# Kernel tuning notes

Measured on AMD Instinct MI355X. Metric: run time of the kernel, lower is better.

The kernel has to match this reference:

```python
import jax, jax.numpy as jnp
import numpy as np

B, T, C, H = 4096, 96, 256, 64  # batch, seq (<= BLOCK_SIZE=96), N_EMBED, head_size


def setup_inputs() -> dict:
    key = jax.random.key(0)
    k1, k2, k3, k4 = jax.random.split(key, 4)
    x = jax.random.normal(k1, (B, T, C), dtype=jnp.float32)
    # nn.Linear(C, H, bias=False) stores W as [H, C]; we keep [C, H] so y = x @ W.
    scale = 1.0 / jnp.sqrt(C)
    Wk = jax.random.normal(k2, (C, H), dtype=jnp.float32) * scale
    Wq = jax.random.normal(k3, (C, H), dtype=jnp.float32) * scale
    Wv = jax.random.normal(k4, (C, H), dtype=jnp.float32) * scale
    return {"x": x, "Wk": Wk, "Wq": Wq, "Wv": Wv}


def reference(x, Wk, Wq, Wv):
    Bx, Tx, Cx = x.shape
    k = x @ Wk                      # [B, T, H]
    q = x @ Wq                      # [B, T, H]
    v = x @ Wv                      # [B, T, H]
    # NOTE: original scales by C**-0.5 (embed dim), not head_size**-0.5.
    wei = jnp.einsum('bth,bsh->bts', q, k) * (Cx ** -0.5)  # [B, T, T]
    causal = jnp.tril(jnp.ones((Tx, Tx), dtype=bool))
    wei = jnp.where(causal, wei, -jnp.inf)
    wei = jax.nn.softmax(wei, axis=-1)
    # dropout is identity at eval time
    return jnp.einsum('bts,bsh->bth', wei, v)  # [B, T, H]
```

## Files before the change

### kernel.cpp

```cpp
#include <hip/hip_runtime.h>
#include <cstddef>


typedef __bf16 bf16x8 __attribute__((ext_vector_type(8)));
typedef float f32x4 __attribute__((ext_vector_type(4)));

static __device__ __forceinline__ unsigned short f2bf_u16(float f) {
  union { float f; unsigned int u; } c; c.f = f;
  return (unsigned short)((c.u + 0x7FFFu + ((c.u >> 16) & 1u)) >> 16);
}

__global__ void pack_w(const float* __restrict__ Wk, const float* __restrict__ Wq,
                       const float* __restrict__ Wv, unsigned short* __restrict__ pack) {
  int idx = blockIdx.x * blockDim.x + threadIdx.x;
  int lane = idx & 63;
  int t = idx >> 6;
  int nt = t & 3; t >>= 2;
  int kt = t & 7; t >>= 3;
  int p  = t;
  if (p >= 3) return;
  const float* W = (p == 0) ? Wk : (p == 1) ? Wq : Wv;
  int k0 = kt * 32 + (lane >> 4) * 8;
  int n  = nt * 16 + (lane & 15);
  unsigned short* dst = pack + (size_t)idx * 8;
#pragma unroll
  for (int j = 0; j < 8; ++j) dst[j] = f2bf_u16(W[(size_t)(k0 + j) * 64 + n]);
}

#define LDQ 72
#define LDV 104
#define LDP 104

__global__ __launch_bounds__(384, 3) void head_fused(
    const float* __restrict__ x, const unsigned short* __restrict__ pack,
    float* __restrict__ out) {
  __shared__ __attribute__((aligned(16))) unsigned short qs [96 * LDQ];
  __shared__ __attribute__((aligned(16))) unsigned short ksm[96 * LDQ];
  __shared__ __attribute__((aligned(16))) unsigned short vTs[64 * LDV];
  __shared__ __attribute__((aligned(16))) unsigned short Ps [96 * LDP];
  __shared__ float rowsum[96];

  const int b    = blockIdx.x;
  const int w    = threadIdx.x >> 6;
  const int lane = threadIdx.x & 63;
  const int lo   = lane & 15;
  const int hi   = lane >> 4;

  const float* __restrict__ xb = x + (size_t)b * (96 * 256);

  f32x4 acc[3][4];
#pragma unroll
  for (int p = 0; p < 3; ++p)
#pragma unroll
    for (int nt = 0; nt < 4; ++nt) acc[p][nt] = (f32x4){0.f, 0.f, 0.f, 0.f};

  const int am = 16 * w + lo;
#pragma unroll 2
  for (int kt = 0; kt < 8; ++kt) {
    const float* src = xb + (size_t)am * 256 + kt * 32 + hi * 8;
    f32x4 a0 = *(const f32x4*)src;
    f32x4 a1 = *(const f32x4*)(src + 4);
    union { bf16x8 v; unsigned short u[8]; } af;
#pragma unroll
    for (int j = 0; j < 4; ++j) { af.u[j] = f2bf_u16(a0[j]); af.u[4 + j] = f2bf_u16(a1[j]); }
#pragma unroll
    for (int p = 0; p < 3; ++p) {
#pragma unroll
      for (int nt = 0; nt < 4; ++nt) {
        bf16x8 bf = *(const bf16x8*)(pack + ((size_t)(((p * 8 + kt) * 4 + nt) * 64 + lane) * 8));
        acc[p][nt] = __builtin_amdgcn_mfma_f32_16x16x32_bf16(af.v, bf, acc[p][nt], 0, 0, 0);
      }
    }
  }
#pragma unroll
  for (int nt = 0; nt < 4; ++nt) {
#pragma unroll
    for (int r = 0; r < 4; ++r) {
      int row = 16 * w + hi * 4 + r;
      int col = 16 * nt + lo;
      ksm[row * LDQ + col] = f2bf_u16(acc[0][nt][r]);
      qs [row * LDQ + col] = f2bf_u16(acc[1][nt][r]);
      vTs[col * LDV + row] = f2bf_u16(acc[2][nt][r]);
    }
  }
  __syncthreads();

  f32x4 sacc[6];
#pragma unroll
  for (int jt = 0; jt < 6; ++jt) sacc[jt] = (f32x4){0.f, 0.f, 0.f, 0.f};

  bf16x8 qf0 = *(const bf16x8*)(qs + (16 * w + lo) * LDQ + hi * 8);
  bf16x8 qf1 = *(const bf16x8*)(qs + (16 * w + lo) * LDQ + 32 + hi * 8);
  for (int jt = 0; jt <= w; ++jt) {
    bf16x8 kf0 = *(const bf16x8*)(ksm + (16 * jt + lo) * LDQ + hi * 8);
    bf16x8 kf1 = *(const bf16x8*)(ksm + (16 * jt + lo) * LDQ + 32 + hi * 8);
    sacc[jt] = __builtin_amdgcn_mfma_f32_16x16x32_bf16(qf0, kf0, sacc[jt], 0, 0, 0);
    sacc[jt] = __builtin_amdgcn_mfma_f32_16x16x32_bf16(qf1, kf1, sacc[jt], 0, 0, 0);
  }

#pragma unroll
  for (int r = 0; r < 4; ++r) {
    int row = 16 * w + hi * 4 + r;
    float pr[6];
    float mx = -1e30f;
    for (int jt = 0; jt <= w; ++jt) {
      int col = 16 * jt + lo;
      float s = sacc[jt][r] * 0.0625f;
      s = (col <= row) ? s : -1e30f;
      pr[jt] = s;
      mx = fmaxf(mx, s);
    }
#pragma unroll
    for (int off = 1; off < 16; off <<= 1) mx = fmaxf(mx, __shfl_xor(mx, off, 64));
    float sum = 0.f;
    for (int jt = 0; jt <= w; ++jt) {
      float p = __expf(pr[jt] - mx);
      pr[jt] = p;
      sum += p;
    }
#pragma unroll
    for (int off = 1; off < 16; off <<= 1) sum += __shfl_xor(sum, off, 64);
#pragma unroll
    for (int jt = 0; jt < 6; ++jt) {
      float p = (jt <= w) ? pr[jt] : 0.f;
      Ps[row * LDP + 16 * jt + lo] = f2bf_u16(p);
    }
    if (lo == 0) rowsum[row] = sum;
  }
  __syncthreads();

  f32x4 oacc[4];
#pragma unroll
  for (int nt = 0; nt < 4; ++nt) oacc[nt] = (f32x4){0.f, 0.f, 0.f, 0.f};

  const int ksmax = (16 * w + 15) >> 5;
  for (int ks = 0; ks <= ksmax; ++ks) {
    bf16x8 pf = *(const bf16x8*)(Ps + (16 * w + lo) * LDP + ks * 32 + hi * 8);
#pragma unroll
    for (int nt = 0; nt < 4; ++nt) {
      bf16x8 vf = *(const bf16x8*)(vTs + (16 * nt + lo) * LDV + ks * 32 + hi * 8);
      oacc[nt] = __builtin_amdgcn_mfma_f32_16x16x32_bf16(pf, vf, oacc[nt], 0, 0, 0);
    }
  }

  float* __restrict__ ob = out + (size_t)b * (96 * 64);
#pragma unroll
  for (int r = 0; r < 4; ++r) {
    int row = 16 * w + hi * 4 + r;
    float inv = 1.0f / rowsum[row];
#pragma unroll
    for (int nt = 0; nt < 4; ++nt) {
      ob[row * 64 + 16 * nt + lo] = oacc[nt][r] * inv;
    }
  }
}

extern "C" void kernel_launch(void* const* d_in, const int* in_sizes, int n_in,
                              void* d_out, int out_size, void* d_ws, size_t ws_size,
                              hipStream_t stream) {
  const float* x  = (const float*)d_in[0];
  const float* Wk = (const float*)d_in[1];
  const float* Wq = (const float*)d_in[2];
  const float* Wv = (const float*)d_in[3];
  float* out = (float*)d_out;
  unsigned short* pack = (unsigned short*)d_ws;

  const int B = in_sizes[0] / (96 * 256);

  pack_w<<<24, 256, 0, stream>>>(Wk, Wq, Wv, pack);
  head_fused<<<B, 384, 0, stream>>>(x, pack, out);
}
```

Before: 689.8 us.

## Split fused attention head into separate QKV-projection and attention kernels

The single fused kernel becomes two launches. The first projects x to Q, K and V, writing Q/K as bf16 into the output buffer and a transposed V into workspace. The second reads them back to compute causal softmax attention. Moving the Q/K/V tiles out of shared memory cuts LDS per block, raising the occupancy bounds (4 and 6 blocks per CU instead of 3) so more memory latency can be hidden. The cost is an extra kernel launch and a global round trip for the intermediates. Reusing the output buffer is safe only because each block reads its own Q/K slice before overwriting it.

Measured after the change: 765.2 us. +10.9%, slower.

```diff
diff --git a/kernel.cpp b/kernel.cpp
--- a/kernel.cpp
+++ b/kernel.cpp
@@ -4,6 +4,7 @@
 
 typedef __bf16 bf16x8 __attribute__((ext_vector_type(8)));
 typedef float f32x4 __attribute__((ext_vector_type(4)));
+typedef unsigned short ushort8 __attribute__((ext_vector_type(8)));
 
 static __device__ __forceinline__ unsigned short f2bf_u16(float f) {
   union { float f; unsigned int u; } c; c.f = f;
@@ -27,18 +28,13 @@
   for (int j = 0; j < 8; ++j) dst[j] = f2bf_u16(W[(size_t)(k0 + j) * 64 + n]);
 }
 
-#define LDQ 72
-#define LDV 104
-#define LDP 104
-
-__global__ __launch_bounds__(384, 3) void head_fused(
+#define LDVA 104
+
+__global__ __launch_bounds__(384, 4) void qkv_kernel(
     const float* __restrict__ x, const unsigned short* __restrict__ pack,
-    float* __restrict__ out) {
-  __shared__ __attribute__((aligned(16))) unsigned short qs [96 * LDQ];
-  __shared__ __attribute__((aligned(16))) unsigned short ksm[96 * LDQ];
-  __shared__ __attribute__((aligned(16))) unsigned short vTs[64 * LDV];
-  __shared__ __attribute__((aligned(16))) unsigned short Ps [96 * LDP];
-  __shared__ float rowsum[96];
+    unsigned short* __restrict__ qk,
+    unsigned short* __restrict__ vT) {
+  __shared__ __attribute__((aligned(16))) unsigned short vTs[64 * LDVA];
 
   const int b    = blockIdx.x;
   const int w    = threadIdx.x >> 6;
@@ -72,28 +68,55 @@
       }
     }
   }
+
+  unsigned short* qb = qk + (size_t)b * 12288;
 #pragma unroll
   for (int nt = 0; nt < 4; ++nt) {
 #pragma unroll
     for (int r = 0; r < 4; ++r) {
       int row = 16 * w + hi * 4 + r;
       int col = 16 * nt + lo;
-      ksm[row * LDQ + col] = f2bf_u16(acc[0][nt][r]);
-      qs [row * LDQ + col] = f2bf_u16(acc[1][nt][r]);
-      vTs[col * LDV + row] = f2bf_u16(acc[2][nt][r]);
+      qb[row * 64 + col]        = f2bf_u16(acc[1][nt][r]);
+      qb[6144 + row * 64 + col] = f2bf_u16(acc[0][nt][r]);
+      vTs[col * LDVA + row]     = f2bf_u16(acc[2][nt][r]);
     }
   }
   __syncthreads();
 
+  unsigned short* vb = vT + (size_t)b * 6144;
+  int h   = threadIdx.x / 6;
+  int seg = threadIdx.x - h * 6;
+  ushort8 s0 = *(const ushort8*)(vTs + h * LDVA + seg * 16);
+  ushort8 s1 = *(const ushort8*)(vTs + h * LDVA + seg * 16 + 8);
+  *(ushort8*)(vb + h * 96 + seg * 16)     = s0;
+  *(ushort8*)(vb + h * 96 + seg * 16 + 8) = s1;
+}
+
+#define LDP 104
+
+__global__ __launch_bounds__(384, 6) void attn_kernel(
+    const unsigned short* qk, const unsigned short* vT, float* out) {
+  __shared__ __attribute__((aligned(16))) unsigned short Ps[96 * LDP];
+  __shared__ float rowsum[96];
+
+  const int b    = blockIdx.x;
+  const int w    = threadIdx.x >> 6;
+  const int lane = threadIdx.x & 63;
+  const int lo   = lane & 15;
+  const int hi   = lane >> 4;
+
+  const unsigned short* qb = qk + (size_t)b * 12288;
+  const unsigned short* kb = qb + 6144;
+
   f32x4 sacc[6];
 #pragma unroll
   for (int jt = 0; jt < 6; ++jt) sacc[jt] = (f32x4){0.f, 0.f, 0.f, 0.f};
 
-  bf16x8 qf0 = *(const bf16x8*)(qs + (16 * w + lo) * LDQ + hi * 8);
-  bf16x8 qf1 = *(const bf16x8*)(qs + (16 * w + lo) * LDQ + 32 + hi * 8);
+  bf16x8 qf0 = *(const bf16x8*)(qb + (16 * w + lo) * 64 + hi * 8);
+  bf16x8 qf1 = *(const bf16x8*)(qb + (16 * w + lo) * 64 + 32 + hi * 8);
   for (int jt = 0; jt <= w; ++jt) {
-    bf16x8 kf0 = *(const bf16x8*)(ksm + (16 * jt + lo) * LDQ + hi * 8);
-    bf16x8 kf1 = *(const bf16x8*)(ksm + (16 * jt + lo) * LDQ + 32 + hi * 8);
+    bf16x8 kf0 = *(const bf16x8*)(kb + (16 * jt + lo) * 64 + hi * 8);
+    bf16x8 kf1 = *(const bf16x8*)(kb + (16 * jt + lo) * 64 + 32 + hi * 8);
     sacc[jt] = __builtin_amdgcn_mfma_f32_16x16x32_bf16(qf0, kf0, sacc[jt], 0, 0, 0);
     sacc[jt] = __builtin_amdgcn_mfma_f32_16x16x32_bf16(qf1, kf1, sacc[jt], 0, 0, 0);
   }
@@ -133,17 +156,18 @@
 #pragma unroll
   for (int nt = 0; nt < 4; ++nt) oacc[nt] = (f32x4){0.f, 0.f, 0.f, 0.f};
 
+  const unsigned short* vb = vT + (size_t)b * 6144;
   const int ksmax = (16 * w + 15) >> 5;
   for (int ks = 0; ks <= ksmax; ++ks) {
     bf16x8 pf = *(const bf16x8*)(Ps + (16 * w + lo) * LDP + ks * 32 + hi * 8);
 #pragma unroll
     for (int nt = 0; nt < 4; ++nt) {
-      bf16x8 vf = *(const bf16x8*)(vTs + (16 * nt + lo) * LDV + ks * 32 + hi * 8);
+      bf16x8 vf = *(const bf16x8*)(vb + (16 * nt + lo) * 96 + ks * 32 + hi * 8);
       oacc[nt] = __builtin_amdgcn_mfma_f32_16x16x32_bf16(pf, vf, oacc[nt], 0, 0, 0);
     }
   }
 
-  float* __restrict__ ob = out + (size_t)b * (96 * 64);
+  float* ob = out + (size_t)b * (96 * 64);
 #pragma unroll
   for (int r = 0; r < 4; ++r) {
     int row = 16 * w + hi * 4 + r;
@@ -163,10 +187,14 @@
   const float* Wq = (const float*)d_in[2];
   const float* Wv = (const float*)d_in[3];
   float* out = (float*)d_out;
+
+  const int B = in_sizes[0] / (96 * 256);
+
   unsigned short* pack = (unsigned short*)d_ws;
-
-  const int B = in_sizes[0] / (96 * 256);
+  unsigned short* vT   = (unsigned short*)((char*)d_ws + 98304);
+  unsigned short* qk   = (unsigned short*)d_out;
 
   pack_w<<<24, 256, 0, stream>>>(Wk, Wq, Wv, pack);
-  head_fused<<<B, 384, 0, stream>>>(x, pack, out);
-}
+  qkv_kernel<<<B, 384, 0, stream>>>(x, pack, qk, vT);
+  attn_kernel<<<B, 384, 0, stream>>>(qk, vT, out);
+}
```

## Process two batches per block and alias shared buffers to cut LDS footprint

Applied to the files above, without the earlier changes.

Each block now handles two batch elements with 768 threads, one half per batch. Shared memory is reduced by reusing buffers: Q and P share one array, and V is held in registers and written transposed into the K buffer after the softmax, at the cost of an extra barrier. The aim is higher occupancy, since LDS per batch element drops. It assumes B is even, and every wave now waits on a block-wide barrier shared by both batches.

Result: no change. 692.9 us (+0.4%).

```diff
diff --git a/kernel.cpp b/kernel.cpp
--- a/kernel.cpp
+++ b/kernel.cpp
@@ -27,26 +27,26 @@
   for (int j = 0; j < 8; ++j) dst[j] = f2bf_u16(W[(size_t)(k0 + j) * 64 + n]);
 }
 
-#define LDQ 72
+#define LDK 72
+#define LDP 104
 #define LDV 104
-#define LDP 104
 
-__global__ __launch_bounds__(384, 3) void head_fused(
+__global__ __launch_bounds__(768, 6) void head_fused(
     const float* __restrict__ x, const unsigned short* __restrict__ pack,
     float* __restrict__ out) {
-  __shared__ __attribute__((aligned(16))) unsigned short qs [96 * LDQ];
-  __shared__ __attribute__((aligned(16))) unsigned short ksm[96 * LDQ];
-  __shared__ __attribute__((aligned(16))) unsigned short vTs[64 * LDV];
-  __shared__ __attribute__((aligned(16))) unsigned short Ps [96 * LDP];
-  __shared__ float rowsum[96];
+  __shared__ __attribute__((aligned(16))) unsigned short ks2[2][96 * LDK];
+  __shared__ __attribute__((aligned(16))) unsigned short SA [2][96 * LDP];
+  __shared__ float rowsum[2][96];
 
-  const int b    = blockIdx.x;
   const int w    = threadIdx.x >> 6;
+  const int half = w >= 6;
+  const int w6   = w - 6 * half;
   const int lane = threadIdx.x & 63;
   const int lo   = lane & 15;
   const int hi   = lane >> 4;
 
-  const float* __restrict__ xb = x + (size_t)b * (96 * 256);
+  const int bb = 2 * blockIdx.x + half;
+  const float* __restrict__ xb = x + (size_t)bb * (96 * 256);
 
   f32x4 acc[3][4];
 #pragma unroll
@@ -54,7 +54,7 @@
 #pragma unroll
     for (int nt = 0; nt < 4; ++nt) acc[p][nt] = (f32x4){0.f, 0.f, 0.f, 0.f};
 
-  const int am = 16 * w + lo;
+  const int am = 16 * w6 + lo;
 #pragma unroll 2
   for (int kt = 0; kt < 8; ++kt) {
     const float* src = xb + (size_t)am * 256 + kt * 32 + hi * 8;
@@ -72,15 +72,17 @@
       }
     }
   }
+
+  unsigned short vv[16];
 #pragma unroll
   for (int nt = 0; nt < 4; ++nt) {
 #pragma unroll
     for (int r = 0; r < 4; ++r) {
-      int row = 16 * w + hi * 4 + r;
+      int row = 16 * w6 + hi * 4 + r;
       int col = 16 * nt + lo;
-      ksm[row * LDQ + col] = f2bf_u16(acc[0][nt][r]);
-      qs [row * LDQ + col] = f2bf_u16(acc[1][nt][r]);
-      vTs[col * LDV + row] = f2bf_u16(acc[2][nt][r]);
+      ks2[half][row * LDK + col] = f2bf_u16(acc[0][nt][r]);
+      SA [half][row * LDP + col] = f2bf_u16(acc[1][nt][r]);
+      vv[nt * 4 + r] = f2bf_u16(acc[2][nt][r]);
     }
   }
   __syncthreads();
@@ -89,21 +91,21 @@
 #pragma unroll
   for (int jt = 0; jt < 6; ++jt) sacc[jt] = (f32x4){0.f, 0.f, 0.f, 0.f};
 
-  bf16x8 qf0 = *(const bf16x8*)(qs + (16 * w + lo) * LDQ + hi * 8);
-  bf16x8 qf1 = *(const bf16x8*)(qs + (16 * w + lo) * LDQ + 32 + hi * 8);
-  for (int jt = 0; jt <= w; ++jt) {
-    bf16x8 kf0 = *(const bf16x8*)(ksm + (16 * jt + lo) * LDQ + hi * 8);
-    bf16x8 kf1 = *(const bf16x8*)(ksm + (16 * jt + lo) * LDQ + 32 + hi * 8);
+  bf16x8 qf0 = *(const bf16x8*)(SA[half] + (16 * w6 + lo) * LDP + hi * 8);
+  bf16x8 qf1 = *(const bf16x8*)(SA[half] + (16 * w6 + lo) * LDP + 32 + hi * 8);
+  for (int jt = 0; jt <= w6; ++jt) {
+    bf16x8 kf0 = *(const bf16x8*)(ks2[half] + (16 * jt + lo) * LDK + hi * 8);
+    bf16x8 kf1 = *(const bf16x8*)(ks2[half] + (16 * jt + lo) * LDK + 32 + hi * 8);
     sacc[jt] = __builtin_amdgcn_mfma_f32_16x16x32_bf16(qf0, kf0, sacc[jt], 0, 0, 0);
     sacc[jt] = __builtin_amdgcn_mfma_f32_16x16x32_bf16(qf1, kf1, sacc[jt], 0, 0, 0);
   }
 
 #pragma unroll
   for (int r = 0; r < 4; ++r) {
-    int row = 16 * w + hi * 4 + r;
+    int row = 16 * w6 + hi * 4 + r;
     float pr[6];
     float mx = -1e30f;
-    for (int jt = 0; jt <= w; ++jt) {
+    for (int jt = 0; jt <= w6; ++jt) {
       int col = 16 * jt + lo;
       float s = sacc[jt][r] * 0.0625f;
       s = (col <= row) ? s : -1e30f;
@@ -113,7 +115,7 @@
 #pragma unroll
     for (int off = 1; off < 16; off <<= 1) mx = fmaxf(mx, __shfl_xor(mx, off, 64));
     float sum = 0.f;
-    for (int jt = 0; jt <= w; ++jt) {
+    for (int jt = 0; jt <= w6; ++jt) {
       float p = __expf(pr[jt] - mx);
       pr[jt] = p;
       sum += p;
@@ -122,10 +124,22 @@
     for (int off = 1; off < 16; off <<= 1) sum += __shfl_xor(sum, off, 64);
 #pragma unroll
     for (int jt = 0; jt < 6; ++jt) {
-      float p = (jt <= w) ? pr[jt] : 0.f;
-      Ps[row * LDP + 16 * jt + lo] = f2bf_u16(p);
+      float p = (jt <= w6) ? pr[jt] : 0.f;
+      SA[half][row * LDP + 16 * jt + lo] = f2bf_u16(p);
     }
-    if (lo == 0) rowsum[row] = sum;
+    if (lo == 0) rowsum[half][row] = sum;
+  }
+  __syncthreads();
+
+  unsigned short* vT = ks2[half];
+#pragma unroll
+  for (int nt = 0; nt < 4; ++nt) {
+#pragma unroll
+    for (int r = 0; r < 4; ++r) {
+      int row = 16 * w6 + hi * 4 + r;
+      int col = 16 * nt + lo;
+      vT[col * LDV + row] = vv[nt * 4 + r];
+    }
   }
   __syncthreads();
 
@@ -133,21 +147,21 @@
 #pragma unroll
   for (int nt = 0; nt < 4; ++nt) oacc[nt] = (f32x4){0.f, 0.f, 0.f, 0.f};
 
-  const int ksmax = (16 * w + 15) >> 5;
+  const int ksmax = (16 * w6 + 15) >> 5;
   for (int ks = 0; ks <= ksmax; ++ks) {
-    bf16x8 pf = *(const bf16x8*)(Ps + (16 * w + lo) * LDP + ks * 32 + hi * 8);
+    bf16x8 pf = *(const bf16x8*)(SA[half] + (16 * w6 + lo) * LDP + ks * 32 + hi * 8);
 #pragma unroll
     for (int nt = 0; nt < 4; ++nt) {
-      bf16x8 vf = *(const bf16x8*)(vTs + (16 * nt + lo) * LDV + ks * 32 + hi * 8);
+      bf16x8 vf = *(const bf16x8*)(vT + (16 * nt + lo) * LDV + ks * 32 + hi * 8);
       oacc[nt] = __builtin_amdgcn_mfma_f32_16x16x32_bf16(pf, vf, oacc[nt], 0, 0, 0);
     }
   }
 
-  float* __restrict__ ob = out + (size_t)b * (96 * 64);
+  float* __restrict__ ob = out + (size_t)bb * (96 * 64);
 #pragma unroll
   for (int r = 0; r < 4; ++r) {
-    int row = 16 * w + hi * 4 + r;
-    float inv = 1.0f / rowsum[row];
+    int row = 16 * w6 + hi * 4 + r;
+    float inv = 1.0f / rowsum[half][row];
 #pragma unroll
     for (int nt = 0; nt < 4; ++nt) {
       ob[row * 64 + 16 * nt + lo] = oacc[nt][r] * inv;
@@ -168,5 +182,5 @@
   const int B = in_sizes[0] / (96 * 256);
 
   pack_w<<<24, 256, 0, stream>>>(Wk, Wq, Wv, pack);
-  head_fused<<<B, 384, 0, stream>>>(x, pack, out);
+  head_fused<<<B / 2, 768, 0, stream>>>(x, pack, out);
 }
```
